# Kernel tuning notes

Hardware: AMD Instinct MI355X
Metric: run time of the kernel (lower is better)

Reference implementation:

```python
import jax, jax.numpy as jnp
import numpy as np

C = 256
B = 8
N = 2048
EPS_BN = 1e-5


def _bn(x, g, b):
    # BatchNorm1d in training mode: stats over (batch, length) per channel
    m = x.mean(axis=(0, 2), keepdims=True)
    v = ((x - m) ** 2).mean(axis=(0, 2), keepdims=True)
    return g[None, :, None] * (x - m) / jnp.sqrt(v + EPS_BN) + b[None, :, None]


def _sa_layer(x, wqk, wv, bv, wt, bt, g, b):
    # shared q/k projection (q_conv.weight = k_conv.weight in the original)
    q = jnp.einsum('oc,bcn->bon', wqk, x)          # [B, C//4, N]
    energy = jnp.einsum('bcm,bcn->bmn', q, q)      # x_q^T x_k -> [B, N, N]
    att = jax.nn.softmax(energy, axis=-1)
    att = att / (1e-9 + att.sum(axis=1, keepdims=True))  # L1 renorm over dim=1
    v = jnp.einsum('oc,bcn->bon', wv, x) + bv[None, :, None]
    x_r = jnp.einsum('bcm,bmn->bcn', v, att)       # [B, C, N]
    t = jnp.einsum('oc,bcn->bon', wt, x - x_r) + bt[None, :, None]
    x_r = jax.nn.relu(_bn(t, g, b))
    return x + x_r


def setup_inputs() -> dict:
    key = jax.random.key(0)
    ks = jax.random.split(key, 16)
    s = lambda k, shp, scale: jax.random.normal(k, shp, dtype=jnp.float32) * scale
    inp = {
        'x': s(ks[0], (B, C, N), 1.0),
        'conv1_w': s(ks[1], (C, C), 1.0 / np.sqrt(C)),
        'conv2_w': s(ks[2], (C, C), 1.0 / np.sqrt(C)),
        'bn1_g': jnp.ones((C,), jnp.float32),
        'bn1_b': jnp.zeros((C,), jnp.float32),
        'bn2_g': jnp.ones((C,), jnp.float32),
        'bn2_b': jnp.zeros((C,), jnp.float32),
        'sa_wqk': s(ks[3], (4, C // 4, C), 1.0 / np.sqrt(C)),
        'sa_wv': s(ks[4], (4, C, C), 1.0 / np.sqrt(C)),
        'sa_bv': s(ks[5], (4, C), 0.01),
        'sa_wt': s(ks[6], (4, C, C), 1.0 / np.sqrt(C)),
        'sa_bt': s(ks[7], (4, C), 0.01),
        'sa_g': jnp.ones((4, C), jnp.float32),
        'sa_b': jnp.zeros((4, C), jnp.float32),
    }
    return inp


def reference(x, conv1_w, conv2_w, bn1_g, bn1_b, bn2_g, bn2_b,
              sa_wqk, sa_wv, sa_bv, sa_wt, sa_bt, sa_g, sa_b):
    x = jax.nn.relu(_bn(jnp.einsum('oc,bcn->bon', conv1_w, x), bn1_g, bn1_b))
    x = jax.nn.relu(_bn(jnp.einsum('oc,bcn->bon', conv2_w, x), bn2_g, bn2_b))
    outs = []
    for i in range(4):  # four structurally identical SA layers, small fixed loop
        x = _sa_layer(x, sa_wqk[i], sa_wv[i], sa_bv[i], sa_wt[i], sa_bt[i],
                      sa_g[i], sa_b[i])
        outs.append(x)
    return jnp.concatenate(outs, axis=1)  # [B, 4*C, N]
```

## Files before the change

kernel.cpp:

```cpp
#include <hip/hip_runtime.h>
#include <hip/hip_bf16.h>

typedef __attribute__((ext_vector_type(8))) short short8;
typedef __attribute__((ext_vector_type(4))) float f32x4;
using bf16 = __hip_bfloat16;

constexpr int C  = 256;
constexpr int BB = 8;
constexpr int NN = 2048;

#define DEVI __device__ __forceinline__

DEVI short8 ldg8(const bf16* p) { return *reinterpret_cast<const short8*>(p); }

DEVI f32x4 mfma16(short8 a, short8 b, f32x4 c) {
  return __builtin_amdgcn_mfma_f32_16x16x32_bf16(a, b, c, 0, 0, 0);
}

DEVI void split2(float x, bf16& h, bf16& l) {
  h = __float2bfloat16(x);
  l = __float2bfloat16(x - __bfloat162float(h));
}

DEVI short b2s(bf16 x) { short s; __builtin_memcpy(&s, &x, 2); return s; }


DEVI void store_tile16(const float v[4], bf16* __restrict__ H, bf16* __restrict__ L,
                       size_t tilebase, float* lds, int lane) {
  int l15 = lane & 15, l4 = lane >> 4;
#pragma unroll
  for (int r = 0; r < 4; ++r) lds[(l4 * 4 + r) * 20 + l15] = v[r];
  asm volatile("s_waitcnt lgkmcnt(0)" ::: "memory");
  __builtin_amdgcn_sched_barrier(0);
  int n = lane & 15, cg = (lane >> 4) & 1, pl = lane >> 5;
  short8 o;
#pragma unroll
  for (int j = 0; j < 8; ++j) {
    bf16 h, l;
    split2(lds[n * 20 + cg * 8 + j], h, l);
    o[j] = pl ? b2s(l) : b2s(h);
  }
  bf16* P = pl ? L : H;
  *reinterpret_cast<short8*>(P + tilebase + (size_t)cg * 128 + n * 8) = o;
}

__global__ __launch_bounds__(256) void k_cvtW(const float* __restrict__ s,
                                              bf16* __restrict__ dh,
                                              bf16* __restrict__ dl, int rows) {
  int idx = blockIdx.x * 256 + threadIdx.x;
  if (idx >= rows * 32) return;
  int row = idx >> 5, kg = idx & 31;
  const float* sp = s + row * 256 + kg * 8;
  short8 oh, ol;
#pragma unroll
  for (int j = 0; j < 8; ++j) {
    bf16 h, l;
    split2(sp[j], h, l);
    oh[j] = b2s(h); ol[j] = b2s(l);
  }
  size_t off = ((size_t)(row >> 4) * 32 + kg) * 128 + (row & 15) * 8;
  *reinterpret_cast<short8*>(dh + off) = oh;
  *reinterpret_cast<short8*>(dl + off) = ol;
}

__global__ __launch_bounds__(256) void k_tin(const float* __restrict__ x,
                                             bf16* __restrict__ Xh,
                                             bf16* __restrict__ Xl) {
  __shared__ float tile[64][65];
  int b = blockIdx.z, n0 = blockIdx.x * 64, c0 = blockIdx.y * 64;
  int t = threadIdx.x;
  int tn = t & 63, tq = t >> 6;
#pragma unroll
  for (int i = 0; i < 16; ++i) {
    int cc = i * 4 + tq;
    tile[cc][tn] = x[((size_t)(b * C + c0 + cc)) * NN + n0 + tn];
  }
  __syncthreads();
  bf16* XHb = Xh + (size_t)b * NN * C;
  bf16* XLb = Xl + (size_t)b * NN * C;
#pragma unroll
  for (int i = 0; i < 4; ++i) {
    int e = i * 256 + t;
    int nl = e & 63;
    int cgp = e >> 6;
    int cg = cgp & 7, pl = cgp >> 3;
    short8 o;
#pragma unroll
    for (int j = 0; j < 8; ++j) {
      bf16 h, l;
      split2(tile[cg * 8 + j][nl], h, l);
      o[j] = pl ? b2s(l) : b2s(h);
    }
    int n = n0 + nl;
    size_t off = ((size_t)(n >> 4) * 32 + ((c0 >> 3) + cg)) * 128 + (n & 15) * 8;
    bf16* P = pl ? XLb : XHb;
    *reinterpret_cast<short8*>(P + off) = o;
  }
}

template <bool OUTF32, bool BIASJ, bool STATS>
__global__ __launch_bounds__(256) void k_gemm_tr(const bf16* __restrict__ Ah,
                                                 const bf16* __restrict__ Al,
                                                 const bf16* __restrict__ Wh,
                                                 const bf16* __restrict__ Wl,
                                                 const float* __restrict__ bias,
                                                 float* __restrict__ OutF,
                                                 bf16* __restrict__ Oh,
                                                 bf16* __restrict__ Ol, int OD,
                                                 float* __restrict__ sS,
                                                 float* __restrict__ sS2) {
  __shared__ float smS[64], smS2[64];
  __shared__ float scratch[4][320];
  int b = blockIdx.x, i0 = blockIdx.y * 64, j0 = blockIdx.z * 64;
  int t = threadIdx.x, lane = t & 63, w = t >> 6;
  int l15 = lane & 15, l4 = lane >> 4;
  if (STATS) {
    if (t < 64) { smS[t] = 0.f; smS2[t] = 0.f; }
    __syncthreads();
  }
  const bf16* Abh = Ah + (size_t)b * NN * C;
  const bf16* Abl = Al + (size_t)b * NN * C;
  int ntile = (i0 >> 4) + w;
  f32x4 acc[4];
#pragma unroll
  for (int ct = 0; ct < 4; ++ct) acc[ct] = f32x4{0.f, 0.f, 0.f, 0.f};
#pragma unroll
  for (int ks = 0; ks < 8; ++ks) {
    int ko = ks * 4 + l4;
    short8 a_h = ldg8(Abh + ((size_t)ntile * 32 + ko) * 128 + l15 * 8);
    short8 a_l = ldg8(Abl + ((size_t)ntile * 32 + ko) * 128 + l15 * 8);
#pragma unroll
    for (int ct = 0; ct < 4; ++ct) {
      size_t wo = ((size_t)((j0 >> 4) + ct) * 32 + ko) * 128 + l15 * 8;
      short8 w_h = ldg8(Wh + wo);
      short8 w_l = ldg8(Wl + wo);
      acc[ct] = mfma16(a_h, w_h, acc[ct]);
      acc[ct] = mfma16(a_h, w_l, acc[ct]);
      acc[ct] = mfma16(a_l, w_h, acc[ct]);
    }
  }
#pragma unroll
  for (int ct = 0; ct < 4; ++ct) {
    float bj = 0.f;
    if (BIASJ) bj = bias[j0 + ct * 16 + l15];
    float v[4];
    float s = 0.f, s2 = 0.f;
#pragma unroll
    for (int r = 0; r < 4; ++r) {
      v[r] = acc[ct][r] + bj;
      if (STATS) { s += v[r]; s2 += v[r] * v[r]; }
    }
    if (OUTF32) {
#pragma unroll
      for (int r = 0; r < 4; ++r) {
        int row = i0 + w * 16 + l4 * 4 + r;
        OutF[((size_t)(b * NN + row)) * OD + j0 + ct * 16 + l15] = v[r];
      }
    } else {
      bf16* Obh = Oh + (size_t)b * NN * OD;
      bf16* Obl = Ol + (size_t)b * NN * OD;
      size_t tb = ((size_t)ntile * (OD >> 3) + ((j0 + ct * 16) >> 3)) * 128;
      store_tile16(v, Obh, Obl, tb, scratch[w], lane);
    }
    if (STATS) {
      s += __shfl_xor(s, 16); s2 += __shfl_xor(s2, 16);
      s += __shfl_xor(s, 32); s2 += __shfl_xor(s2, 32);
      if (l4 == 0) {
        atomicAdd(&smS[ct * 16 + l15], s);
        atomicAdd(&smS2[ct * 16 + l15], s2);
      }
    }
  }
  if (STATS) {
    __syncthreads();
    if (t < 64) {
      atomicAdd(&sS[j0 + t], smS[t]);
      atomicAdd(&sS2[j0 + t], smS2[t]);
    }
  }
}

__global__ __launch_bounds__(256) void k_qproj(const bf16* __restrict__ Xh,
                                               const bf16* __restrict__ Xl,
                                               const bf16* __restrict__ Wh,
                                               const bf16* __restrict__ Wl,
                                               bf16* __restrict__ Qh,
                                               bf16* __restrict__ Ql) {
  __shared__ float scratch[4][320];
  int b = blockIdx.x, ntile = blockIdx.y;
  int t = threadIdx.x, lane = t & 63, w = t >> 6;
  int l15 = lane & 15, l4 = lane >> 4;
  const bf16* Abh = Xh + (size_t)b * NN * C;
  const bf16* Abl = Xl + (size_t)b * NN * C;
  f32x4 acc = {0.f, 0.f, 0.f, 0.f};
#pragma unroll
  for (int ks = 0; ks < 8; ++ks) {
    int ko = ks * 4 + l4;
    short8 a_h = ldg8(Abh + ((size_t)ntile * 32 + ko) * 128 + l15 * 8);
    short8 a_l = ldg8(Abl + ((size_t)ntile * 32 + ko) * 128 + l15 * 8);
    size_t wo = ((size_t)w * 32 + ko) * 128 + l15 * 8;
    short8 w_h = ldg8(Wh + wo);
    short8 w_l = ldg8(Wl + wo);
    acc = mfma16(a_h, w_h, acc);
    acc = mfma16(a_h, w_l, acc);
    acc = mfma16(a_l, w_h, acc);
  }
  float v[4] = {acc[0], acc[1], acc[2], acc[3]};
  size_t tb = ((size_t)ntile * 8 + w * 2) * 128;
  store_tile16(v, Qh + (size_t)b * NN * 64, Ql + (size_t)b * NN * 64, tb,
               scratch[w], lane);
}

__global__ __launch_bounds__(256) void k_gemm_nm(const bf16* __restrict__ Wh,
                                                 const bf16* __restrict__ Wl,
                                                 const bf16* __restrict__ Xh,
                                                 const bf16* __restrict__ Xl,
                                                 const float* __restrict__ bias,
                                                 bf16* __restrict__ Vh,
                                                 bf16* __restrict__ Vl) {
  __shared__ float scratch[4][320];
  int b = blockIdx.x, i0 = blockIdx.y * 64, j0 = blockIdx.z * 64;
  int t = threadIdx.x, lane = t & 63, w = t >> 6;
  int l15 = lane & 15, l4 = lane >> 4;
  const bf16* Xbh = Xh + (size_t)b * NN * C;
  const bf16* Xbl = Xl + (size_t)b * NN * C;
  int ntile = (i0 >> 4) + w;
  f32x4 acc[4];
#pragma unroll
  for (int ct = 0; ct < 4; ++ct) acc[ct] = f32x4{0.f, 0.f, 0.f, 0.f};
#pragma unroll
  for (int ks = 0; ks < 8; ++ks) {
    int ko = ks * 4 + l4;
    short8 a_h = ldg8(Wh + ((size_t)ntile * 32 + ko) * 128 + l15 * 8);
    short8 a_l = ldg8(Wl + ((size_t)ntile * 32 + ko) * 128 + l15 * 8);
#pragma unroll
    for (int ct = 0; ct < 4; ++ct) {
      size_t xo = ((size_t)((j0 >> 4) + ct) * 32 + ko) * 128 + l15 * 8;
      short8 x_h = ldg8(Xbh + xo);
      short8 x_l = ldg8(Xbl + xo);
      acc[ct] = mfma16(a_h, x_h, acc[ct]);
      acc[ct] = mfma16(a_h, x_l, acc[ct]);
      acc[ct] = mfma16(a_l, x_h, acc[ct]);
    }
  }
  float br[4];
#pragma unroll
  for (int r = 0; r < 4; ++r) br[r] = bias[i0 + w * 16 + l4 * 4 + r];
  bf16* Vbh = Vh + (size_t)b * C * NN;
  bf16* Vbl = Vl + (size_t)b * C * NN;
#pragma unroll
  for (int ct = 0; ct < 4; ++ct) {
    float v[4];
#pragma unroll
    for (int r = 0; r < 4; ++r) v[r] = acc[ct][r] + br[r];
    size_t tb = ((size_t)ntile * (NN >> 3) + ((j0 + ct * 16) >> 3)) * 128;
    store_tile16(v, Vbh, Vbl, tb, scratch[w], lane);
  }
}

__global__ __launch_bounds__(256) void k_rowstats(const bf16* __restrict__ Qh,
                                                  const bf16* __restrict__ Ql,
                                                  float* __restrict__ rm,
                                                  float* __restrict__ irs) {
  __shared__ float redM[4][16], redS[4][16];
  int b = blockIdx.x;
  int t = threadIdx.x, lane = t & 63, w = t >> 6;
  int l15 = lane & 15, l4 = lane >> 4;
  int mt = blockIdx.y;
  const bf16* QHb = Qh + (size_t)b * NN * 64;
  const bf16* QLb = Ql + (size_t)b * NN * 64;
  short8 ah0 = ldg8(QHb + ((size_t)mt * 8 + l4) * 128 + l15 * 8);
  short8 ah1 = ldg8(QHb + ((size_t)mt * 8 + 4 + l4) * 128 + l15 * 8);
  short8 al0 = ldg8(QLb + ((size_t)mt * 8 + l4) * 128 + l15 * 8);
  short8 al1 = ldg8(QLb + ((size_t)mt * 8 + 4 + l4) * 128 + l15 * 8);
  float lmax[4], lsum[4];
#pragma unroll
  for (int r = 0; r < 4; ++r) { lmax[r] = -3.4e38f; lsum[r] = 0.f; }
  for (int nb = w * 32; nb < w * 32 + 32; ++nb) {
    short8 bh0 = ldg8(QHb + ((size_t)nb * 8 + l4) * 128 + l15 * 8);
    short8 bh1 = ldg8(QHb + ((size_t)nb * 8 + 4 + l4) * 128 + l15 * 8);
    short8 bl0 = ldg8(QLb + ((size_t)nb * 8 + l4) * 128 + l15 * 8);
    short8 bl1 = ldg8(QLb + ((size_t)nb * 8 + 4 + l4) * 128 + l15 * 8);
    f32x4 e = {0.f, 0.f, 0.f, 0.f};
    e = mfma16(ah0, bh0, e); e = mfma16(ah1, bh1, e);
    e = mfma16(ah0, bl0, e); e = mfma16(ah1, bl1, e);
    e = mfma16(al0, bh0, e); e = mfma16(al1, bh1, e);
#pragma unroll
    for (int r = 0; r < 4; ++r) {
      float v = e[r];
      float nm = fmaxf(lmax[r], v);
      lsum[r] = lsum[r] * __expf(lmax[r] - nm) + __expf(v - nm);
      lmax[r] = nm;
    }
  }
#pragma unroll
  for (int r = 0; r < 4; ++r) {
    for (int mk = 1; mk < 16; mk <<= 1) {
      float om = __shfl_xor(lmax[r], mk, 16);
      float os = __shfl_xor(lsum[r], mk, 16);
      float nm = fmaxf(lmax[r], om);
      lsum[r] = lsum[r] * __expf(lmax[r] - nm) + os * __expf(om - nm);
      lmax[r] = nm;
    }
  }
  if (l15 == 0) {
#pragma unroll
    for (int r = 0; r < 4; ++r) {
      redM[w][l4 * 4 + r] = lmax[r];
      redS[w][l4 * 4 + r] = lsum[r];
    }
  }
  __syncthreads();
  if (t < 16) {
    float m = redM[0][t];
    m = fmaxf(m, redM[1][t]); m = fmaxf(m, redM[2][t]); m = fmaxf(m, redM[3][t]);
    float s = 0.f;
#pragma unroll
    for (int w2 = 0; w2 < 4; ++w2) s += redS[w2][t] * __expf(redM[w2][t] - m);
    rm[b * NN + mt * 16 + t] = m;
    irs[b * NN + mt * 16 + t] = 1.0f / s;
  }
}

__global__ __launch_bounds__(512, 4) void k_attnY(const bf16* __restrict__ QH,
                                                  const bf16* __restrict__ QL,
                                                  const bf16* __restrict__ VH,
                                                  const bf16* __restrict__ VL,
                                                  const float* __restrict__ rm,
                                                  const float* __restrict__ irs,
                                                  const float* __restrict__ Xf,
                                                  bf16* __restrict__ DH,
                                                  bf16* __restrict__ DL) {
  __shared__ bf16 Pb[2][32 * 136];
  __shared__ float rmL[2048], irL[2048];
  __shared__ float colLds[32];
  __shared__ float scratch[8][320];
  int bid = blockIdx.x;
  int b = bid & 7, n0 = (bid >> 3) * 32;
  int t = threadIdx.x, lane = t & 63, w = t >> 6;
  int l15 = lane & 15, l4 = lane >> 4;
  int nt = w >> 2, pp = w & 3;
  const bf16* QHb = QH + (size_t)b * NN * 64;
  const bf16* QLb = QL + (size_t)b * NN * 64;
  const bf16* VHb = VH + (size_t)b * C * NN;
  const bf16* VLb = VL + (size_t)b * C * NN;
  for (int i = t; i < NN; i += 512) {
    rmL[i] = rm[b * NN + i];
    irL[i] = irs[b * NN + i];
  }
  if (t < 32) colLds[t] = 0.f;
  int ntq = (n0 >> 4) + nt;
  short8 qh0 = ldg8(QHb + ((size_t)ntq * 8 + l4) * 128 + l15 * 8);
  short8 qh1 = ldg8(QHb + ((size_t)ntq * 8 + 4 + l4) * 128 + l15 * 8);
  short8 ql0 = ldg8(QLb + ((size_t)ntq * 8 + l4) * 128 + l15 * 8);
  short8 ql1 = ldg8(QLb + ((size_t)ntq * 8 + 4 + l4) * 128 + l15 * 8);
  f32x4 zero = {0.f, 0.f, 0.f, 0.f};
  f32x4 acc[2][2];
#pragma unroll
  for (int a = 0; a < 2; ++a)
#pragma unroll
    for (int ct = 0; ct < 2; ++ct) acc[a][ct] = zero;
  float cac[4] = {0.f, 0.f, 0.f, 0.f};
  __syncthreads();
  for (int s = 0; s < 16; ++s) {
    bf16* pbw = Pb[s & 1];
#pragma unroll
    for (int sub = 0; sub < 2; ++sub) {
      int mt8 = pp * 2 + sub;
      int gmt = s * 8 + mt8;
      short8 bh0 = ldg8(QHb + ((size_t)gmt * 8 + l4) * 128 + l15 * 8);
      short8 bh1 = ldg8(QHb + ((size_t)gmt * 8 + 4 + l4) * 128 + l15 * 8);
      short8 bl0 = ldg8(QLb + ((size_t)gmt * 8 + l4) * 128 + l15 * 8);
      short8 bl1 = ldg8(QLb + ((size_t)gmt * 8 + 4 + l4) * 128 + l15 * 8);
      f32x4 eA = zero, eB = zero;
      eA = mfma16(qh0, bh0, eA); eB = mfma16(qh1, bh1, eB);
      eA = mfma16(qh0, bl0, eA); eB = mfma16(qh1, bl1, eB);
      eA = mfma16(ql0, bh0, eA); eB = mfma16(ql1, bh1, eB);
      float rmv = rmL[gmt * 16 + l15], iv = irL[gmt * 16 + l15];
      int blk = nt * 16 + mt8 * 2 + (l15 >> 3);
#pragma unroll
      for (int r = 0; r < 4; ++r) {
        float p = __expf(eA[r] + eB[r] - rmv) * iv;
        bf16 ph = __float2bfloat16(p);
        cac[r] += __bfloat162float(ph);
        pbw[blk * 136 + (l4 * 4 + r) * 8 + (l15 & 7)] = ph;
      }
    }
    short8 vhA[2][2], vlA[2][2];
#pragma unroll
    for (int kc = 0; kc < 2; ++kc)
#pragma unroll
      for (int ct = 0; ct < 2; ++ct) {
        size_t vo = ((size_t)(w * 2 + ct) * 256 + s * 16 + kc * 4 + l4) * 128 + l15 * 8;
        vhA[kc][ct] = ldg8(VHb + vo);
        vlA[kc][ct] = ldg8(VLb + vo);
      }
    asm volatile("s_waitcnt lgkmcnt(0)" ::: "memory");
    __builtin_amdgcn_sched_barrier(0);
    __builtin_amdgcn_s_barrier();
    short8 vhB[2][2], vlB[2][2];
#pragma unroll
    for (int kc = 0; kc < 2; ++kc)
#pragma unroll
      for (int ct = 0; ct < 2; ++ct) {
        size_t vo = ((size_t)(w * 2 + ct) * 256 + s * 16 + (kc + 2) * 4 + l4) * 128 + l15 * 8;
        vhB[kc][ct] = ldg8(VHb + vo);
        vlB[kc][ct] = ldg8(VLb + vo);
      }
#pragma unroll
    for (int kc = 0; kc < 2; ++kc) {
      short8 pa0 = *reinterpret_cast<const short8*>(&pbw[(kc * 4 + l4) * 136 + l15 * 8]);
      short8 pa1 = *reinterpret_cast<const short8*>(&pbw[(16 + kc * 4 + l4) * 136 + l15 * 8]);
#pragma unroll
      for (int ct = 0; ct < 2; ++ct) {
        acc[0][ct] = mfma16(pa0, vhA[kc][ct], acc[0][ct]);
        acc[0][ct] = mfma16(pa0, vlA[kc][ct], acc[0][ct]);
        acc[1][ct] = mfma16(pa1, vhA[kc][ct], acc[1][ct]);
        acc[1][ct] = mfma16(pa1, vlA[kc][ct], acc[1][ct]);
      }
    }
#pragma unroll
    for (int kc = 0; kc < 2; ++kc) {
      short8 pa0 = *reinterpret_cast<const short8*>(&pbw[((kc + 2) * 4 + l4) * 136 + l15 * 8]);
      short8 pa1 = *reinterpret_cast<const short8*>(&pbw[(16 + (kc + 2) * 4 + l4) * 136 + l15 * 8]);
#pragma unroll
      for (int ct = 0; ct < 2; ++ct) {
        acc[0][ct] = mfma16(pa0, vhB[kc][ct], acc[0][ct]);
        acc[0][ct] = mfma16(pa0, vlB[kc][ct], acc[0][ct]);
        acc[1][ct] = mfma16(pa1, vhB[kc][ct], acc[1][ct]);
        acc[1][ct] = mfma16(pa1, vlB[kc][ct], acc[1][ct]);
      }
    }
  }
#pragma unroll
  for (int r = 0; r < 4; ++r) {
    float v2 = cac[r];
    v2 += __shfl_xor(v2, 1, 16); v2 += __shfl_xor(v2, 2, 16);
    v2 += __shfl_xor(v2, 4, 16); v2 += __shfl_xor(v2, 8, 16);
    if (l15 == 0) atomicAdd(&colLds[nt * 16 + l4 * 4 + r], v2);
  }
  __syncthreads();
  if (t < 32) colLds[t] = 1.0f / (1e-9f + colLds[t]);
  __syncthreads();
  bf16* DHb = DH + (size_t)b * NN * C;
  bf16* DLb = DL + (size_t)b * NN * C;
#pragma unroll
  for (int a = 0; a < 2; ++a) {
#pragma unroll
    for (int ct = 0; ct < 2; ++ct) {
      float d[4];
      int cidx = w * 32 + ct * 16 + l15;
#pragma unroll
      for (int r = 0; r < 4; ++r) {
        int n = n0 + a * 16 + l4 * 4 + r;
        d[r] = Xf[((size_t)(b * NN + n)) * C + cidx] -
               acc[a][ct][r] * colLds[a * 16 + l4 * 4 + r];
      }
      size_t tb = ((size_t)((n0 >> 4) + a) * 32 + ((w * 32 + ct * 16) >> 3)) * 128;
      store_tile16(d, DHb, DLb, tb, scratch[w], lane);
    }
  }
}

__global__ void k_bnfin(const float* __restrict__ sS, const float* __restrict__ sS2,
                        const float* __restrict__ g, const float* __restrict__ bb,
                        float* __restrict__ scale, float* __restrict__ shift) {
  int c = threadIdx.x;
  float cnt = (float)(BB * NN);
  float mean = sS[c] / cnt;
  float var = fmaxf(sS2[c] / cnt - mean * mean, 0.f);
  float sc = g[c] * rsqrtf(var + 1e-5f);
  scale[c] = sc;
  shift[c] = bb[c] - mean * sc;
}

template <bool RES>
__global__ __launch_bounds__(256) void k_bnrelu(const float* __restrict__ Tt,
                                                const float* __restrict__ scale,
                                                const float* __restrict__ shift,
                                                float* __restrict__ Xf,
                                                bf16* __restrict__ Xh,
                                                bf16* __restrict__ Xl,
                                                float* __restrict__ outp, int Loff) {
  __shared__ float vb[16][257];
  int b = blockIdx.x, n0 = blockIdx.y * 16;
  int c = threadIdx.x;
  float sc = scale[c], sh = shift[c];
#pragma unroll
  for (int i = 0; i < 16; ++i) {
    int n = n0 + i;
    size_t idx = ((size_t)(b * NN + n)) * C + c;
    float v = Tt[idx] * sc + sh;
    v = fmaxf(v, 0.f);
    if (RES) v += Xf[idx];
    Xf[idx] = v;
    bf16 h, l;
    split2(v, h, l);
    size_t off = (size_t)b * NN * C +
                 ((size_t)(n >> 4) * 32 + (c >> 3)) * 128 + (n & 15) * 8 + (c & 7);
    Xh[off] = h;
    Xl[off] = l;
    if (RES) vb[i][c] = v;
  }
  if (RES) {
    __syncthreads();
    int nl = threadIdx.x & 15, cb = threadIdx.x >> 4;
#pragma unroll
    for (int j = 0; j < 16; ++j) {
      int cc = cb + j * 16;
      outp[((size_t)(b * 1024 + Loff + cc)) * NN + n0 + nl] = vb[nl][cc];
    }
  }
}

extern "C" void kernel_launch(void* const* d_in, const int* in_sizes, int n_in,
                              void* d_out, int out_size, void* d_ws, size_t ws_size,
                              hipStream_t stream) {
  const float* x       = (const float*)d_in[0];
  const float* conv1_w = (const float*)d_in[1];
  const float* conv2_w = (const float*)d_in[2];
  const float* bn1_g   = (const float*)d_in[3];
  const float* bn1_b   = (const float*)d_in[4];
  const float* bn2_g   = (const float*)d_in[5];
  const float* bn2_b   = (const float*)d_in[6];
  const float* wqk     = (const float*)d_in[7];
  const float* wv      = (const float*)d_in[8];
  const float* bv      = (const float*)d_in[9];
  const float* wt      = (const float*)d_in[10];
  const float* bt      = (const float*)d_in[11];
  const float* sg      = (const float*)d_in[12];
  const float* sb      = (const float*)d_in[13];
  float* out = (float*)d_out;

  char* p = (char*)d_ws;
  auto take = [&](size_t n) { char* r = p; p += n; return r; };
  bf16* WB1h = (bf16*)take(131072);
  bf16* WB1l = (bf16*)take(131072);
  bf16* WB2h = (bf16*)take(131072);
  bf16* WB2l = (bf16*)take(131072);
  bf16* WBQh = (bf16*)take(131072);
  bf16* WBQl = (bf16*)take(131072);
  bf16* WBVh = (bf16*)take(524288);
  bf16* WBVl = (bf16*)take(524288);
  bf16* WBTh = (bf16*)take(524288);
  bf16* WBTl = (bf16*)take(524288);
  bf16* XTh  = (bf16*)take(8388608);
  bf16* XTl  = (bf16*)take(8388608);
  float* XF  = (float*)take(16777216);
  bf16* QTh  = (bf16*)take(2097152);
  bf16* QTl  = (bf16*)take(2097152);
  bf16* VBh  = (bf16*)take(8388608);
  bf16* VBl  = (bf16*)take(8388608);
  float* TT  = (float*)VBh;
  bf16* DTh  = (bf16*)take(8388608);
  bf16* DTl  = (bf16*)take(8388608);
  float* RM   = (float*)take(65536);
  float* IRS  = (float*)take(65536);
  float* STAT = (float*)take(12288);
  float* SCSH = (float*)take(12288);

  hipMemsetAsync(STAT, 0, 6 * 512 * sizeof(float), stream);
  k_cvtW<<<32, 256, 0, stream>>>(conv1_w, WB1h, WB1l, 256);
  k_cvtW<<<32, 256, 0, stream>>>(conv2_w, WB2h, WB2l, 256);
  k_cvtW<<<32, 256, 0, stream>>>(wqk, WBQh, WBQl, 256);
  k_cvtW<<<128, 256, 0, stream>>>(wv, WBVh, WBVl, 1024);
  k_cvtW<<<128, 256, 0, stream>>>(wt, WBTh, WBTl, 1024);
  k_tin<<<dim3(32, 4, 8), 256, 0, stream>>>(x, XTh, XTl);

  k_gemm_tr<true, false, true><<<dim3(8, 32, 4), 256, 0, stream>>>(
      XTh, XTl, WB1h, WB1l, nullptr, TT, nullptr, nullptr, 256, STAT + 0, STAT + 256);
  k_bnfin<<<1, 256, 0, stream>>>(STAT + 0, STAT + 256, bn1_g, bn1_b, SCSH + 0, SCSH + 256);
  k_bnrelu<false><<<dim3(8, 128), 256, 0, stream>>>(TT, SCSH + 0, SCSH + 256, XF, XTh, XTl,
                                                    nullptr, 0);

  k_gemm_tr<true, false, true><<<dim3(8, 32, 4), 256, 0, stream>>>(
      XTh, XTl, WB2h, WB2l, nullptr, TT, nullptr, nullptr, 256, STAT + 512, STAT + 768);
  k_bnfin<<<1, 256, 0, stream>>>(STAT + 512, STAT + 768, bn2_g, bn2_b, SCSH + 512, SCSH + 768);
  k_bnrelu<false><<<dim3(8, 128), 256, 0, stream>>>(TT, SCSH + 512, SCSH + 768, XF, XTh, XTl,
                                                    nullptr, 0);

  for (int L = 0; L < 4; ++L) {
    float* ST = STAT + (2 + L) * 512;
    float* SC = SCSH + (2 + L) * 512;
    k_qproj<<<dim3(8, 128), 256, 0, stream>>>(XTh, XTl, WBQh + L * 16384,
                                              WBQl + L * 16384, QTh, QTl);
    k_gemm_nm<<<dim3(8, 4, 32), 256, 0, stream>>>(WBVh + L * 65536, WBVl + L * 65536,
                                                  XTh, XTl, bv + L * 256, VBh, VBl);
    k_rowstats<<<dim3(8, 128), 256, 0, stream>>>(QTh, QTl, RM, IRS);
    k_attnY<<<512, 512, 0, stream>>>(QTh, QTl, VBh, VBl, RM, IRS, XF, DTh, DTl);
    k_gemm_tr<true, true, true><<<dim3(8, 32, 4), 256, 0, stream>>>(
        DTh, DTl, WBTh + L * 65536, WBTl + L * 65536, bt + L * 256, TT, nullptr, nullptr,
        256, ST, ST + 256);
    k_bnfin<<<1, 256, 0, stream>>>(ST, ST + 256, sg + L * 256, sb + L * 256, SC, SC + 256);
    k_bnrelu<true><<<dim3(8, 128), 256, 0, stream>>>(TT, SC, SC + 256, XF, XTh, XTl, out,
                                                     L * 256);
  }
}
```

Before: 680.4 us.

## Double attention query tile to 64 and use two-pass row stats

k_attnY now handles 64 query columns per block instead of 32, so each V tile loaded from global memory feeds four accumulator rows rather than two. This halves V re-reads and the grid size, at the cost of more registers and LDS (occupancy hint lowered from 4 to 2) and fewer blocks per GPU. k_rowstats is restructured into two passes: a plain max, then a sum of exps. This replaces the online-softmax rescaling, and the energies are recomputed in the second pass. Each block of k_rowstats now covers 4 row tiles using 8 warps.

```diff
diff --git a/kernel.cpp b/kernel.cpp
--- a/kernel.cpp
+++ b/kernel.cpp
@@ -258,71 +258,85 @@
   }
 }
 
-__global__ __launch_bounds__(256) void k_rowstats(const bf16* __restrict__ Qh,
+__global__ __launch_bounds__(512) void k_rowstats(const bf16* __restrict__ Qh,
                                                   const bf16* __restrict__ Ql,
                                                   float* __restrict__ rm,
                                                   float* __restrict__ irs) {
-  __shared__ float redM[4][16], redS[4][16];
+  __shared__ float redM[8][16], redS[8][16];
   int b = blockIdx.x;
   int t = threadIdx.x, lane = t & 63, w = t >> 6;
   int l15 = lane & 15, l4 = lane >> 4;
-  int mt = blockIdx.y;
+  int nt = w >> 1, pp = w & 1;
+  int mt = blockIdx.y * 4 + nt;
   const bf16* QHb = Qh + (size_t)b * NN * 64;
   const bf16* QLb = Ql + (size_t)b * NN * 64;
   short8 ah0 = ldg8(QHb + ((size_t)mt * 8 + l4) * 128 + l15 * 8);
   short8 ah1 = ldg8(QHb + ((size_t)mt * 8 + 4 + l4) * 128 + l15 * 8);
   short8 al0 = ldg8(QLb + ((size_t)mt * 8 + l4) * 128 + l15 * 8);
   short8 al1 = ldg8(QLb + ((size_t)mt * 8 + 4 + l4) * 128 + l15 * 8);
-  float lmax[4], lsum[4];
-#pragma unroll
-  for (int r = 0; r < 4; ++r) { lmax[r] = -3.4e38f; lsum[r] = 0.f; }
-  for (int nb = w * 32; nb < w * 32 + 32; ++nb) {
+  f32x4 zero = {0.f, 0.f, 0.f, 0.f};
+  float lmax[4];
+#pragma unroll
+  for (int r = 0; r < 4; ++r) lmax[r] = -3.4e38f;
+  for (int nb = pp * 64; nb < pp * 64 + 64; ++nb) {
     short8 bh0 = ldg8(QHb + ((size_t)nb * 8 + l4) * 128 + l15 * 8);
     short8 bh1 = ldg8(QHb + ((size_t)nb * 8 + 4 + l4) * 128 + l15 * 8);
     short8 bl0 = ldg8(QLb + ((size_t)nb * 8 + l4) * 128 + l15 * 8);
     short8 bl1 = ldg8(QLb + ((size_t)nb * 8 + 4 + l4) * 128 + l15 * 8);
-    f32x4 e = {0.f, 0.f, 0.f, 0.f};
+    f32x4 e = zero;
     e = mfma16(ah0, bh0, e); e = mfma16(ah1, bh1, e);
     e = mfma16(ah0, bl0, e); e = mfma16(ah1, bl1, e);
     e = mfma16(al0, bh0, e); e = mfma16(al1, bh1, e);
 #pragma unroll
-    for (int r = 0; r < 4; ++r) {
-      float v = e[r];
-      float nm = fmaxf(lmax[r], v);
-      lsum[r] = lsum[r] * __expf(lmax[r] - nm) + __expf(v - nm);
-      lmax[r] = nm;
-    }
+    for (int r = 0; r < 4; ++r) lmax[r] = fmaxf(lmax[r], e[r]);
   }
 #pragma unroll
   for (int r = 0; r < 4; ++r) {
-    for (int mk = 1; mk < 16; mk <<= 1) {
-      float om = __shfl_xor(lmax[r], mk, 16);
-      float os = __shfl_xor(lsum[r], mk, 16);
-      float nm = fmaxf(lmax[r], om);
-      lsum[r] = lsum[r] * __expf(lmax[r] - nm) + os * __expf(om - nm);
-      lmax[r] = nm;
-    }
+    for (int mk = 1; mk < 16; mk <<= 1)
+      lmax[r] = fmaxf(lmax[r], __shfl_xor(lmax[r], mk, 16));
   }
   if (l15 == 0) {
 #pragma unroll
-    for (int r = 0; r < 4; ++r) {
-      redM[w][l4 * 4 + r] = lmax[r];
-      redS[w][l4 * 4 + r] = lsum[r];
-    }
+    for (int r = 0; r < 4; ++r) redM[w][l4 * 4 + r] = lmax[r];
   }
   __syncthreads();
-  if (t < 16) {
-    float m = redM[0][t];
-    m = fmaxf(m, redM[1][t]); m = fmaxf(m, redM[2][t]); m = fmaxf(m, redM[3][t]);
-    float s = 0.f;
-#pragma unroll
-    for (int w2 = 0; w2 < 4; ++w2) s += redS[w2][t] * __expf(redM[w2][t] - m);
-    rm[b * NN + mt * 16 + t] = m;
-    irs[b * NN + mt * 16 + t] = 1.0f / s;
-  }
-}
-
-__global__ __launch_bounds__(512, 4) void k_attnY(const bf16* __restrict__ QH,
+  float rmv[4];
+#pragma unroll
+  for (int r = 0; r < 4; ++r)
+    rmv[r] = fmaxf(redM[nt * 2][l4 * 4 + r], redM[nt * 2 + 1][l4 * 4 + r]);
+  float lsum[4] = {0.f, 0.f, 0.f, 0.f};
+  for (int nb = pp * 64; nb < pp * 64 + 64; ++nb) {
+    short8 bh0 = ldg8(QHb + ((size_t)nb * 8 + l4) * 128 + l15 * 8);
+    short8 bh1 = ldg8(QHb + ((size_t)nb * 8 + 4 + l4) * 128 + l15 * 8);
+    short8 bl0 = ldg8(QLb + ((size_t)nb * 8 + l4) * 128 + l15 * 8);
+    short8 bl1 = ldg8(QLb + ((size_t)nb * 8 + 4 + l4) * 128 + l15 * 8);
+    f32x4 e = zero;
+    e = mfma16(ah0, bh0, e); e = mfma16(ah1, bh1, e);
+    e = mfma16(ah0, bl0, e); e = mfma16(ah1, bl1, e);
+    e = mfma16(al0, bh0, e); e = mfma16(al1, bh1, e);
+#pragma unroll
+    for (int r = 0; r < 4; ++r) lsum[r] += __expf(e[r] - rmv[r]);
+  }
+#pragma unroll
+  for (int r = 0; r < 4; ++r) {
+    for (int mk = 1; mk < 16; mk <<= 1) lsum[r] += __shfl_xor(lsum[r], mk, 16);
+  }
+  if (l15 == 0) {
+#pragma unroll
+    for (int r = 0; r < 4; ++r) redS[w][l4 * 4 + r] = lsum[r];
+  }
+  __syncthreads();
+  if (t < 64) {
+    int nt2 = t >> 4, row = t & 15;
+    float mx = fmaxf(redM[nt2 * 2][row], redM[nt2 * 2 + 1][row]);
+    float s = redS[nt2 * 2][row] + redS[nt2 * 2 + 1][row];
+    int m = blockIdx.y * 64 + t;
+    rm[b * NN + m] = mx;
+    irs[b * NN + m] = 1.0f / s;
+  }
+}
+
+__global__ __launch_bounds__(512, 2) void k_attnY(const bf16* __restrict__ QH,
                                                   const bf16* __restrict__ QL,
                                                   const bf16* __restrict__ VH,
                                                   const bf16* __restrict__ VL,
@@ -331,15 +345,15 @@
                                                   const float* __restrict__ Xf,
                                                   bf16* __restrict__ DH,
                                                   bf16* __restrict__ DL) {
-  __shared__ bf16 Pb[2][32 * 136];
+  __shared__ bf16 Pb[2][64 * 136];
   __shared__ float rmL[2048], irL[2048];
-  __shared__ float colLds[32];
+  __shared__ float colLds[64];
   __shared__ float scratch[8][320];
   int bid = blockIdx.x;
-  int b = bid & 7, n0 = (bid >> 3) * 32;
+  int b = bid & 7, n0 = (bid >> 3) * 64;
   int t = threadIdx.x, lane = t & 63, w = t >> 6;
   int l15 = lane & 15, l4 = lane >> 4;
-  int nt = w >> 2, pp = w & 3;
+  int nt = w >> 1, pp = w & 1;
   const bf16* QHb = QH + (size_t)b * NN * 64;
   const bf16* QLb = QL + (size_t)b * NN * 64;
   const bf16* VHb = VH + (size_t)b * C * NN;
@@ -348,16 +362,16 @@
     rmL[i] = rm[b * NN + i];
     irL[i] = irs[b * NN + i];
   }
-  if (t < 32) colLds[t] = 0.f;
+  if (t < 64) colLds[t] = 0.f;
   int ntq = (n0 >> 4) + nt;
   short8 qh0 = ldg8(QHb + ((size_t)ntq * 8 + l4) * 128 + l15 * 8);
   short8 qh1 = ldg8(QHb + ((size_t)ntq * 8 + 4 + l4) * 128 + l15 * 8);
   short8 ql0 = ldg8(QLb + ((size_t)ntq * 8 + l4) * 128 + l15 * 8);
   short8 ql1 = ldg8(QLb + ((size_t)ntq * 8 + 4 + l4) * 128 + l15 * 8);
   f32x4 zero = {0.f, 0.f, 0.f, 0.f};
-  f32x4 acc[2][2];
-#pragma unroll
-  for (int a = 0; a < 2; ++a)
+  f32x4 acc[4][2];
+#pragma unroll
+  for (int a = 0; a < 4; ++a)
 #pragma unroll
     for (int ct = 0; ct < 2; ++ct) acc[a][ct] = zero;
   float cac[4] = {0.f, 0.f, 0.f, 0.f};
@@ -365,8 +379,8 @@
   for (int s = 0; s < 16; ++s) {
     bf16* pbw = Pb[s & 1];
 #pragma unroll
-    for (int sub = 0; sub < 2; ++sub) {
-      int mt8 = pp * 2 + sub;
+    for (int sub = 0; sub < 4; ++sub) {
+      int mt8 = pp * 4 + sub;
       int gmt = s * 8 + mt8;
       short8 bh0 = ldg8(QHb + ((size_t)gmt * 8 + l4) * 128 + l15 * 8);
       short8 bh1 = ldg8(QHb + ((size_t)gmt * 8 + 4 + l4) * 128 + l15 * 8);
@@ -409,27 +423,32 @@
       }
 #pragma unroll
     for (int kc = 0; kc < 2; ++kc) {
-      short8 pa0 = *reinterpret_cast<const short8*>(&pbw[(kc * 4 + l4) * 136 + l15 * 8]);
-      short8 pa1 = *reinterpret_cast<const short8*>(&pbw[(16 + kc * 4 + l4) * 136 + l15 * 8]);
-#pragma unroll
-      for (int ct = 0; ct < 2; ++ct) {
-        acc[0][ct] = mfma16(pa0, vhA[kc][ct], acc[0][ct]);
-        acc[0][ct] = mfma16(pa0, vlA[kc][ct], acc[0][ct]);
-        acc[1][ct] = mfma16(pa1, vhA[kc][ct], acc[1][ct]);
-        acc[1][ct] = mfma16(pa1, vlA[kc][ct], acc[1][ct]);
-      }
+      short8 pa[4];
+#pragma unroll
+      for (int a = 0; a < 4; ++a)
+        pa[a] = *reinterpret_cast<const short8*>(&pbw[(a * 16 + kc * 4 + l4) * 136 + l15 * 8]);
+#pragma unroll
+      for (int ct = 0; ct < 2; ++ct)
+#pragma unroll
+        for (int a = 0; a < 4; ++a) {
+          acc[a][ct] = mfma16(pa[a], vhA[kc][ct], acc[a][ct]);
+          acc[a][ct] = mfma16(pa[a], vlA[kc][ct], acc[a][ct]);
+        }
     }
 #pragma unroll
     for (int kc = 0; kc < 2; ++kc) {
-      short8 pa0 = *reinterpret_cast<const short8*>(&pbw[((kc + 2) * 4 + l4) * 136 + l15 * 8]);
-      short8 pa1 = *reinterpret_cast<const short8*>(&pbw[(16 + (kc + 2) * 4 + l4) * 136 + l15 * 8]);
-#pragma unroll
-      for (int ct = 0; ct < 2; ++ct) {
-        acc[0][ct] = mfma16(pa0, vhB[kc][ct], acc[0][ct]);
-        acc[0][ct] = mfma16(pa0, vlB[kc][ct], acc[0][ct]);
-        acc[1][ct] = mfma16(pa1, vhB[kc][ct], acc[1][ct]);
-        acc[1][ct] = mfma16(pa1, vlB[kc][ct], acc[1][ct]);
-      }
+      short8 pa[4];
+#pragma unroll
+      for (int a = 0; a < 4; ++a)
+        pa[a] = *reinterpret_cast<const short8*>(
+            &pbw[(a * 16 + (kc + 2) * 4 + l4) * 136 + l15 * 8]);
+#pragma unroll
+      for (int ct = 0; ct < 2; ++ct)
+#pragma unroll
+        for (int a = 0; a < 4; ++a) {
+          acc[a][ct] = mfma16(pa[a], vhB[kc][ct], acc[a][ct]);
+          acc[a][ct] = mfma16(pa[a], vlB[kc][ct], acc[a][ct]);
+        }
     }
   }
 #pragma unroll
@@ -440,12 +459,12 @@
     if (l15 == 0) atomicAdd(&colLds[nt * 16 + l4 * 4 + r], v2);
   }
   __syncthreads();
-  if (t < 32) colLds[t] = 1.0f / (1e-9f + colLds[t]);
+  if (t < 64) colLds[t] = 1.0f / (1e-9f + colLds[t]);
   __syncthreads();
   bf16* DHb = DH + (size_t)b * NN * C;
   bf16* DLb = DL + (size_t)b * NN * C;
 #pragma unroll
-  for (int a = 0; a < 2; ++a) {
+  for (int a = 0; a < 4; ++a) {
 #pragma unroll
     for (int ct = 0; ct < 2; ++ct) {
       float d[4];
@@ -586,8 +605,8 @@
                                               WBQl + L * 16384, QTh, QTl);
     k_gemm_nm<<<dim3(8, 4, 32), 256, 0, stream>>>(WBVh + L * 65536, WBVl + L * 65536,
                                                   XTh, XTl, bv + L * 256, VBh, VBl);
-    k_rowstats<<<dim3(8, 128), 256, 0, stream>>>(QTh, QTl, RM, IRS);
-    k_attnY<<<512, 512, 0, stream>>>(QTh, QTl, VBh, VBl, RM, IRS, XF, DTh, DTl);
+    k_rowstats<<<dim3(8, 32), 512, 0, stream>>>(QTh, QTl, RM, IRS);
+    k_attnY<<<256, 512, 0, stream>>>(QTh, QTl, VBh, VBl, RM, IRS, XF, DTh, DTl);
     k_gemm_tr<true, true, true><<<dim3(8, 32, 4), 256, 0, stream>>>(
         DTh, DTl, WBTh + L * 65536, WBTl + L * 65536, bt + L * 256, TT, nullptr, nullptr,
         256, ST, ST + 256);
```

New measurement: 759.8 us. 11.7% more time.
